# Kernel tuning notes

Hardware: AMD Instinct MI355X
Metric: run time of the kernel (lower is better)

Reference implementation:

```python
import jax, jax.numpy as jnp
import numpy as np

B, S, D_IN, D_OUT = 8, 2048, 768, 768

def setup_inputs() -> dict:
    key = jax.random.key(0)
    k1, k2 = jax.random.split(key)
    x = jax.random.normal(k1, (B, S, D_IN), dtype=jnp.float32)
    QKV = jax.random.normal(k2, (3, D_IN, D_OUT), dtype=jnp.float32) * 0.02
    return {"x": x, "QKV": QKV}

def reference(x, QKV):
    # Single-head self-attention; scale uses sqrt(d_in) as in the original.
    q = jnp.einsum('bsd,de->bse', x, QKV[0])  # [B,S,D_OUT]
    k = jnp.einsum('bsd,de->bse', x, QKV[1])
    v = jnp.einsum('bsd,de->bse', x, QKV[2])
    scale = 1.0 / jnp.sqrt(jnp.asarray(x.shape[-1], dtype=x.dtype))
    scores = jnp.einsum('bqe,bke->bqk', q, k) * scale  # [B,S,S]
    probs = jax.nn.softmax(scores, axis=-1)
    return jnp.einsum('bqk,bke->bqe', probs, v)  # [B,S,D_OUT]
```

## Files before the change

### kernel.cpp

```cpp
#include <hip/hip_runtime.h>
#include <hip/hip_bf16.h>
#include <cstdint>


#define NB 8
#define NS 2048
#define ND 768
#define NQK 1536
#define MTOT 16384

using f32x4 = __attribute__((ext_vector_type(4))) float;
using s16x8 = __attribute__((ext_vector_type(8))) short;

struct alignas(16) bf16x8 { __hip_bfloat16 h[8]; };
struct alignas(8)  bf16x4 { __hip_bfloat16 h[4]; };

#define CVT_BLOCKS 4096
#define WT_BLOCKS 1728
__global__ __launch_bounds__(256) void preprocess_kernel(const float* __restrict__ x,
                                                         __hip_bfloat16* __restrict__ xb,
                                                         const float* __restrict__ W,
                                                         __hip_bfloat16* __restrict__ Wt,
                                                         float* __restrict__ rowsum) {
    __shared__ float tile[32][33];
    const int tid = threadIdx.x;
    if (blockIdx.x < CVT_BLOCKS) {
#pragma unroll
        for (int it = 0; it < 3; ++it) {
            const int i = (it * CVT_BLOCKS + blockIdx.x) * 256 + tid;
            const f32x4 v = __builtin_nontemporal_load((const f32x4*)x + i);
            bf16x4 o;
            o.h[0] = __float2bfloat16(v[0]);
            o.h[1] = __float2bfloat16(v[1]);
            o.h[2] = __float2bfloat16(v[2]);
            o.h[3] = __float2bfloat16(v[3]);
            ((bf16x4*)xb)[i] = o;
        }
    } else if (blockIdx.x < CVT_BLOCKS + WT_BLOCKS) {
        const int bid = blockIdx.x - CVT_BLOCKS;
        const int e = bid / 576, rem = bid % 576;
        const int k0 = (rem / 24) * 32, n0 = (rem % 24) * 32;
        const float* Wp = W + (size_t)e * ND * ND;
        __hip_bfloat16* Wo = Wt + (size_t)e * ND * ND;
        {
            const int ty = tid >> 3, tx = tid & 7;
            const f32x4 v = __builtin_nontemporal_load(
                (const f32x4*)&Wp[(k0 + ty) * ND + n0 + tx * 4]);
#pragma unroll
            for (int q = 0; q < 4; ++q) tile[ty][tx * 4 + q] = v[q];
        }
        __syncthreads();
        {
            const int np = tid >> 3, kq = tid & 7;
            bf16x4 o;
#pragma unroll
            for (int q = 0; q < 4; ++q) o.h[q] = __float2bfloat16(tile[kq * 4 + q][np]);
            *(bf16x4*)&Wo[(long)(n0 + np) * ND + k0 + kq * 4] = o;
        }
    } else {
        const int i = (blockIdx.x - CVT_BLOCKS - WT_BLOCKS) * 1024 + tid * 4;
        f32x4 z = {0.f, 0.f, 0.f, 0.f};
        *(f32x4*)(rowsum + i) = z;
    }
}

__device__ __forceinline__ void storeC(float* p, float v) { *p = v; }
__device__ __forceinline__ void storeC(__hip_bfloat16* p, float v) { *p = __float2bfloat16(v); }

template <typename OutT, int EPI, bool BATCH_X>
__global__ __launch_bounds__(256, 3) void gemm_bt_kernel(
    const __hip_bfloat16* __restrict__ A,
    const __hip_bfloat16* __restrict__ Bm,
    OutT* __restrict__ C,
    __hip_bfloat16* __restrict__ vtOut,
    float* __restrict__ rowsum,
    int K, int lda, int ldb, int ldc,
    long sA, long sB, long sC, float scale) {
    __shared__ char smem[32768];
    char* AsB = smem;
    char* BsB = smem + 16384;

    int b, tileM, tileN;
    if (BATCH_X) {
        b = blockIdx.x; tileN = blockIdx.y * 128; tileM = blockIdx.z * 128;
    } else {
        b = blockIdx.z; tileN = blockIdx.x * 128; tileM = blockIdx.y * 128;
    }
    A  += (long)b * sA;
    Bm += (long)b * sB;
    C  += (long)b * sC;

    const int tid  = threadIdx.x;
    const int lane = tid & 63;
    const int wave = tid >> 6;
    const int wm = (wave >> 1) * 64;
    const int wn = (wave & 1) * 64;
    const int quad = lane >> 4;
    const int lrow = lane & 15;

    const int srow = tid >> 3;
    const int scol = ((tid & 7) ^ (srow & 7)) << 3;

    f32x4 acc[4][4];
    const f32x4 zero = {0.f, 0.f, 0.f, 0.f};
#pragma unroll
    for (int i = 0; i < 4; ++i)
#pragma unroll
        for (int j = 0; j < 4; ++j) acc[i][j] = zero;

    const __hip_bfloat16* gA = A + (long)(tileM + srow) * lda + scol;
    const __hip_bfloat16* gB = Bm + (long)(tileN + srow) * ldb + scol;
    const int ldsOff = tid * 16;

    typedef const __attribute__((address_space(1))) void* gp;
    typedef __attribute__((address_space(3))) void* sp;

    const int swa = (lrow & 7) << 4;

    for (int k0 = 0; k0 < K; k0 += 64) {
        __syncthreads();
#pragma unroll
        for (int j = 0; j < 4; ++j)
            __builtin_amdgcn_global_load_lds((gp)(gA + (long)(j * 32) * lda + k0),
                                             (sp)(AsB + j * 4096 + ldsOff), 16, 0, 0);
#pragma unroll
        for (int j = 0; j < 4; ++j)
            __builtin_amdgcn_global_load_lds((gp)(gB + (long)(j * 32) * ldb + k0),
                                             (sp)(BsB + j * 4096 + ldsOff), 16, 0, 0);
        __syncthreads();

#pragma unroll
        for (int kk = 0; kk < 2; ++kk) {
            s16x8 af[4], bfr[4];
#pragma unroll
            for (int i = 0; i < 4; ++i)
                af[i] = *(const s16x8*)(AsB + (wm + i * 16 + lrow) * 128 +
                                        ((((kk << 2) | quad) << 4) ^ swa));
#pragma unroll
            for (int j = 0; j < 4; ++j)
                bfr[j] = *(const s16x8*)(BsB + (wn + j * 16 + lrow) * 128 +
                                         ((((kk << 2) | quad) << 4) ^ swa));
#pragma unroll
            for (int i = 0; i < 4; ++i)
#pragma unroll
                for (int j = 0; j < 4; ++j)
                    acc[i][j] = __builtin_amdgcn_mfma_f32_16x16x32_bf16(af[i], bfr[j], acc[i][j], 0, 0, 0);
        }
    }

    if (EPI == 2 && tileN >= NQK) {
        __syncthreads();
        char* T = smem;
#pragma unroll
        for (int i = 0; i < 4; ++i) {
#pragma unroll
            for (int j = 0; j < 4; ++j) {
                const int d = wn + j * 16 + lrow;
                const int s = wm + i * 16 + quad * 4;
                bf16x4 g;
#pragma unroll
                for (int r = 0; r < 4; ++r) g.h[r] = __float2bfloat16(acc[i][j][r]);
                const int c = s >> 3;
                const int off = d * 256 + (((c ^ (d & 15)) << 4) | ((s & 4) << 1));
                *(bf16x4*)(T + off) = g;
            }
        }
        __syncthreads();
        const int dl = tid >> 1, half = tid & 1;
        const long bb = tileM >> 11;
        const int s0 = tileM & (NS - 1);
        const long dg = (long)(tileN - NQK) + dl;
        __hip_bfloat16* dst = vtOut + (bb * ND + dg) * NS + s0;
#pragma unroll
        for (int cc = 0; cc < 8; ++cc) {
            const int c2 = half * 8 + cc;
            s16x8 val = *(const s16x8*)(T + dl * 256 + ((c2 ^ (dl & 15)) << 4));
            *(s16x8*)(dst + c2 * 8) = val;
        }
        return;
    }

    if (EPI == 3) {
#pragma unroll
        for (int i = 0; i < 4; ++i) {
            float rs[4] = {0.f, 0.f, 0.f, 0.f};
#pragma unroll
            for (int j = 0; j < 4; ++j) {
                const int col = tileN + wn + j * 16 + lrow;
#pragma unroll
                for (int r = 0; r < 4; ++r) {
                    const int row = tileM + wm + i * 16 + quad * 4 + r;
                    const float e = __expf(acc[i][j][r] * scale);
                    const __hip_bfloat16 h = __float2bfloat16(e);
                    storeC(C + (long)row * ldc + col, __bfloat162float(h));
                    rs[r] += __bfloat162float(h);
                }
            }
#pragma unroll
            for (int r = 0; r < 4; ++r) {
#pragma unroll
                for (int off = 1; off < 16; off <<= 1) rs[r] += __shfl_xor(rs[r], off);
            }
            if (lrow == 0) {
#pragma unroll
                for (int r = 0; r < 4; ++r)
                    atomicAdd(rowsum + (long)b * NS + tileM + wm + i * 16 + quad * 4 + r, rs[r]);
            }
        }
        return;
    }

    if (EPI == 4) {
#pragma unroll
        for (int i = 0; i < 4; ++i) {
            float inv[4];
#pragma unroll
            for (int r = 0; r < 4; ++r)
                inv[r] = 1.0f / rowsum[(long)b * NS + tileM + wm + i * 16 + quad * 4 + r];
#pragma unroll
            for (int j = 0; j < 4; ++j) {
                const int col = tileN + wn + j * 16 + lrow;
#pragma unroll
                for (int r = 0; r < 4; ++r) {
                    const int row = tileM + wm + i * 16 + quad * 4 + r;
                    storeC(C + (long)row * ldc + col, acc[i][j][r] * inv[r]);
                }
            }
        }
        return;
    }

#pragma unroll
    for (int i = 0; i < 4; ++i) {
#pragma unroll
        for (int j = 0; j < 4; ++j) {
            const int col = tileN + wn + j * 16 + lrow;
#pragma unroll
            for (int r = 0; r < 4; ++r) {
                const int row = tileM + wm + i * 16 + quad * 4 + r;
                storeC(C + (long)row * ldc + col, acc[i][j][r] * scale);
            }
        }
    }
}

extern "C" void kernel_launch(void* const* d_in, const int* in_sizes, int n_in,
                              void* d_out, int out_size, void* d_ws, size_t ws_size,
                              hipStream_t stream) {
    const float* x   = (const float*)d_in[0];
    const float* QKV = (const float*)d_in[1];
    float* out = (float*)d_out;

    uint8_t* ws = (uint8_t*)d_ws;
    constexpr size_t XB_BYTES  = (size_t)MTOT * ND * 2;
    constexpr size_t WT_BYTES  = (size_t)3 * ND * ND * 2;
    constexpr size_t QKV_BYTES = (size_t)MTOT * NQK * 2;
    constexpr size_t VT_BYTES  = (size_t)NB * ND * NS * 2;
    constexpr size_t PR_BYTES  = (size_t)MTOT * NS * 2;
    __hip_bfloat16* xb    = (__hip_bfloat16*)(ws);
    __hip_bfloat16* Wt    = (__hip_bfloat16*)(ws + XB_BYTES);
    __hip_bfloat16* qkvb  = (__hip_bfloat16*)(ws + XB_BYTES + WT_BYTES);
    __hip_bfloat16* vt    = (__hip_bfloat16*)(ws + XB_BYTES + WT_BYTES + QKV_BYTES);
    __hip_bfloat16* probs = (__hip_bfloat16*)(ws + XB_BYTES + WT_BYTES + QKV_BYTES + VT_BYTES);
    float*          rowsum= (float*)(ws + XB_BYTES + WT_BYTES + QKV_BYTES + VT_BYTES + PR_BYTES);

    const float scale = 0.03608439182435161f;

    preprocess_kernel<<<CVT_BLOCKS + WT_BLOCKS + 16, 256, 0, stream>>>(x, xb, QKV, Wt, rowsum);
    gemm_bt_kernel<__hip_bfloat16, 2, false><<<dim3(2304 / 128, MTOT / 128, 1), 256, 0, stream>>>(
        xb, Wt, qkvb, vt, nullptr, ND, ND, ND, NQK, 0, 0, 0, 1.0f);
    gemm_bt_kernel<__hip_bfloat16, 3, true><<<dim3(NB, NS / 128, NS / 128), 256, 0, stream>>>(
        qkvb, qkvb + ND, probs, nullptr, rowsum, ND, NQK, NQK, NS,
        (long)NS * NQK, (long)NS * NQK, (long)NS * NS, scale);
    gemm_bt_kernel<float, 4, true><<<dim3(NB, ND / 128, NS / 128), 256, 0, stream>>>(
        probs, vt, out, nullptr, rowsum, NS, NS, NS, ND,
        (long)NS * NS, (long)ND * NS, (long)NS * ND, 1.0f);
}
```

Baseline: 286.2 us.

## Replace 128x128 GEMM with 256x256 double-buffered pipelined 8-wave kernel

All three GEMMs now use 256x256 tiles computed by 512 threads, with 128KB LDS double buffering. Async global-to-LDS loads for the next K-tiles are interleaved with MFMA quarters using explicit waitcnt, s_barrier and setprio scheduling. The QKV projection also remaps blocks into eight interleaved groups to improve L2 locality. This targets exposed load latency and per-tile synchronisation overhead, at the cost of higher register pressure, one block per CU-class occupancy, and fewer blocks (e.g. 192 for the PV GEMM), which can leave the GPU underfilled.

```diff
diff --git a/kernel.cpp b/kernel.cpp
--- a/kernel.cpp
+++ b/kernel.cpp
@@ -67,24 +67,114 @@
 __device__ __forceinline__ void storeC(float* p, float v) { *p = v; }
 __device__ __forceinline__ void storeC(__hip_bfloat16* p, float v) { *p = __float2bfloat16(v); }
 
-template <typename OutT, int EPI, bool BATCH_X>
-__global__ __launch_bounds__(256, 3) void gemm_bt_kernel(
+typedef const __attribute__((address_space(1))) void* gp;
+typedef __attribute__((address_space(3))) void* sp;
+
+#define SBAR() asm volatile("s_barrier" ::: "memory")
+
+#define STAGE_AH(H_, T_) do {                                                              \
+    char* d_ = smem + (((T_) & 1) * 65536) + (H_) * 16384 + ldsOff;                        \
+    __builtin_amdgcn_global_load_lds((gp)(gA + (long)((H_) * 128) * lda + (T_) * 64),      \
+                                     (sp)d_, 16, 0, 0);                                    \
+    __builtin_amdgcn_global_load_lds((gp)(gA + (long)((H_) * 128 + 64) * lda + (T_) * 64), \
+                                     (sp)(d_ + 8192), 16, 0, 0);                           \
+} while (0)
+
+#define STAGE_BH(H_, T_) do {                                                              \
+    char* d_ = smem + (((T_) & 1) * 65536) + 32768 + (H_) * 16384 + ldsOff;                \
+    __builtin_amdgcn_global_load_lds((gp)(gB + (long)((H_) * 128) * ldb + (T_) * 64),      \
+                                     (sp)d_, 16, 0, 0);                                    \
+    __builtin_amdgcn_global_load_lds((gp)(gB + (long)((H_) * 128 + 64) * ldb + (T_) * 64), \
+                                     (sp)(d_ + 8192), 16, 0, 0);                           \
+} while (0)
+
+#define MFMA_Q(MI0_, NI0_) do {                                                            \
+    _Pragma("unroll") for (int m_ = 0; m_ < 4; ++m_)                                       \
+    _Pragma("unroll") for (int n_ = 0; n_ < 2; ++n_)                                       \
+    _Pragma("unroll") for (int k_ = 0; k_ < 2; ++k_)                                       \
+        acc[(MI0_) + m_][(NI0_) + n_] = __builtin_amdgcn_mfma_f32_16x16x32_bf16(           \
+            af[m_][k_], bf[(NI0_) + n_][k_], acc[(MI0_) + m_][(NI0_) + n_], 0, 0, 0);      \
+} while (0)
+
+#define KTILE(T_, SP1_, SP3_, SP4_, VM_) do {                                              \
+    char* abase = smem + (((T_) & 1) * 65536);                                             \
+    char* bbase = abase + 32768;                                                           \
+                  \
+    _Pragma("unroll") for (int m_ = 0; m_ < 4; ++m_) {                                     \
+        af[m_][0] = *(const s16x8*)(abase + aoff + m_ * 2048 + ck0);                       \
+        af[m_][1] = *(const s16x8*)(abase + aoff + m_ * 2048 + ck1);                       \
+    }                                                                                      \
+    _Pragma("unroll") for (int n_ = 0; n_ < 2; ++n_) {                                     \
+        bf[n_][0] = *(const s16x8*)(bbase + boff + n_ * 2048 + ck0);                       \
+        bf[n_][1] = *(const s16x8*)(bbase + boff + n_ * 2048 + ck1);                       \
+    }                                                                                      \
+    if (SP1_) STAGE_AH(1, (T_) + 1);                                                       \
+    asm volatile("s_waitcnt lgkmcnt(8)" ::: "memory");                                     \
+    SBAR();                                                                                \
+    asm volatile("s_waitcnt lgkmcnt(0)" ::: "memory");                                     \
+    __builtin_amdgcn_sched_barrier(0);                                                     \
+    __builtin_amdgcn_s_setprio(1);                                                         \
+    MFMA_Q(0, 0);                                                                          \
+    __builtin_amdgcn_s_setprio(0);                                                         \
+    SBAR();                                                                                \
+           \
+    _Pragma("unroll") for (int n_ = 0; n_ < 2; ++n_) {                                     \
+        bf[2 + n_][0] = *(const s16x8*)(bbase + boff + (2 + n_) * 2048 + ck0);             \
+        bf[2 + n_][1] = *(const s16x8*)(bbase + boff + (2 + n_) * 2048 + ck1);             \
+    }                                                                                      \
+    SBAR();                                                                                \
+    asm volatile("s_waitcnt lgkmcnt(0)" ::: "memory");                                     \
+    __builtin_amdgcn_sched_barrier(0);                                                     \
+    __builtin_amdgcn_s_setprio(1);                                                         \
+    MFMA_Q(0, 2);                                                                          \
+    __builtin_amdgcn_s_setprio(0);                                                         \
+    SBAR();                                                                                \
+           \
+    _Pragma("unroll") for (int m_ = 0; m_ < 4; ++m_) {                                     \
+        af[m_][0] = *(const s16x8*)(abase + aoff + (4 + m_) * 2048 + ck0);                 \
+        af[m_][1] = *(const s16x8*)(abase + aoff + (4 + m_) * 2048 + ck1);                 \
+    }                                                                                      \
+    if (SP3_) STAGE_BH(0, (T_) + 2);                                                       \
+    SBAR();                                                                                \
+    asm volatile("s_waitcnt lgkmcnt(0)" ::: "memory");                                     \
+    __builtin_amdgcn_sched_barrier(0);                                                     \
+    __builtin_amdgcn_s_setprio(1);                                                         \
+    MFMA_Q(4, 2);                                                                          \
+    __builtin_amdgcn_s_setprio(0);                                                         \
+    SBAR();                                                                                \
+            \
+    if (SP4_) { STAGE_AH(0, (T_) + 2); STAGE_BH(1, (T_) + 2); }                            \
+    if ((VM_) == 0) { asm volatile("s_waitcnt vmcnt(6)" ::: "memory"); }                   \
+    else if ((VM_) == 1) { asm volatile("s_waitcnt vmcnt(0)" ::: "memory"); }              \
+    SBAR();                                                                                \
+    __builtin_amdgcn_s_setprio(1);                                                         \
+    MFMA_Q(4, 0);                                                                          \
+    __builtin_amdgcn_s_setprio(0);                                                         \
+    SBAR();                                                                                \
+} while (0)
+
+template <typename OutT, int EPI, int NKT, bool BATCH_X>
+__global__ __launch_bounds__(512, 2) void gemm256_kernel(
     const __hip_bfloat16* __restrict__ A,
     const __hip_bfloat16* __restrict__ Bm,
     OutT* __restrict__ C,
     __hip_bfloat16* __restrict__ vtOut,
     float* __restrict__ rowsum,
-    int K, int lda, int ldb, int ldc,
+    int lda, int ldb, int ldc,
     long sA, long sB, long sC, float scale) {
-    __shared__ char smem[32768];
-    char* AsB = smem;
-    char* BsB = smem + 16384;
+    static_assert(NKT >= 3, "pipeline needs >= 3 K-tiles");
+    __shared__ alignas(16) char smem[131072];
 
     int b, tileM, tileN;
     if (BATCH_X) {
-        b = blockIdx.x; tileN = blockIdx.y * 128; tileM = blockIdx.z * 128;
+        b = blockIdx.x; tileN = blockIdx.y * 256; tileM = blockIdx.z * 256;
     } else {
-        b = blockIdx.z; tileN = blockIdx.x * 128; tileM = blockIdx.y * 128;
+        b = 0;
+        const int l0 = blockIdx.y * gridDim.x + blockIdx.x;
+        const int cpx = (gridDim.x * gridDim.y) >> 3;
+        const int tl = (l0 & 7) * cpx + (l0 >> 3);
+        tileN = (tl % gridDim.x) * 256;
+        tileM = (tl / gridDim.x) * 256;
     }
     A  += (long)b * sA;
     Bm += (long)b * sB;
@@ -92,76 +182,55 @@
 
     const int tid  = threadIdx.x;
     const int lane = tid & 63;
-    const int wave = tid >> 6;
-    const int wm = (wave >> 1) * 64;
-    const int wn = (wave & 1) * 64;
+    const int wid  = tid >> 6;
+    const int wr   = wid >> 2;
+    const int wc   = wid & 3;
     const int quad = lane >> 4;
     const int lrow = lane & 15;
 
     const int srow = tid >> 3;
     const int scol = ((tid & 7) ^ (srow & 7)) << 3;
-
-    f32x4 acc[4][4];
-    const f32x4 zero = {0.f, 0.f, 0.f, 0.f};
-#pragma unroll
-    for (int i = 0; i < 4; ++i)
-#pragma unroll
-        for (int j = 0; j < 4; ++j) acc[i][j] = zero;
-
     const __hip_bfloat16* gA = A + (long)(tileM + srow) * lda + scol;
     const __hip_bfloat16* gB = Bm + (long)(tileN + srow) * ldb + scol;
     const int ldsOff = tid * 16;
 
-    typedef const __attribute__((address_space(1))) void* gp;
-    typedef __attribute__((address_space(3))) void* sp;
-
-    const int swa = (lrow & 7) << 4;
-
-    for (int k0 = 0; k0 < K; k0 += 64) {
-        __syncthreads();
-#pragma unroll
-        for (int j = 0; j < 4; ++j)
-            __builtin_amdgcn_global_load_lds((gp)(gA + (long)(j * 32) * lda + k0),
-                                             (sp)(AsB + j * 4096 + ldsOff), 16, 0, 0);
-#pragma unroll
-        for (int j = 0; j < 4; ++j)
-            __builtin_amdgcn_global_load_lds((gp)(gB + (long)(j * 32) * ldb + k0),
-                                             (sp)(BsB + j * 4096 + ldsOff), 16, 0, 0);
-        __syncthreads();
-
-#pragma unroll
-        for (int kk = 0; kk < 2; ++kk) {
-            s16x8 af[4], bfr[4];
-#pragma unroll
-            for (int i = 0; i < 4; ++i)
-                af[i] = *(const s16x8*)(AsB + (wm + i * 16 + lrow) * 128 +
-                                        ((((kk << 2) | quad) << 4) ^ swa));
-#pragma unroll
-            for (int j = 0; j < 4; ++j)
-                bfr[j] = *(const s16x8*)(BsB + (wn + j * 16 + lrow) * 128 +
-                                         ((((kk << 2) | quad) << 4) ^ swa));
-#pragma unroll
-            for (int i = 0; i < 4; ++i)
-#pragma unroll
-                for (int j = 0; j < 4; ++j)
-                    acc[i][j] = __builtin_amdgcn_mfma_f32_16x16x32_bf16(af[i], bfr[j], acc[i][j], 0, 0, 0);
-        }
-    }
+    const int swa  = lrow & 7;
+    const int ck0  = (quad ^ swa) << 4;
+    const int ck1  = ((quad + 4) ^ swa) << 4;
+    const int aoff = wr * 16384 + lrow * 128;
+    const int boff = wc * 8192 + lrow * 128;
+
+    f32x4 acc[8][4];
+    const f32x4 zero = {0.f, 0.f, 0.f, 0.f};
+#pragma unroll
+    for (int i = 0; i < 8; ++i)
+#pragma unroll
+        for (int j = 0; j < 4; ++j) acc[i][j] = zero;
+
+    STAGE_AH(0, 0); STAGE_BH(0, 0); STAGE_BH(1, 0); STAGE_AH(1, 0);
+    asm volatile("s_waitcnt vmcnt(4)" ::: "memory");
+    STAGE_AH(0, 1); STAGE_BH(0, 1); STAGE_BH(1, 1);
+    asm volatile("s_waitcnt vmcnt(6)" ::: "memory");
+    SBAR();
+
+    s16x8 af[4][2], bf[4][2];
+#pragma unroll 1
+    for (int t = 0; t < NKT - 2; ++t) { KTILE(t, 1, 1, 1, 0); }
+    KTILE(NKT - 2, 1, 0, 0, 1);
+    KTILE(NKT - 1, 0, 0, 0, 2);
 
     if (EPI == 2 && tileN >= NQK) {
-        __syncthreads();
         char* T = smem;
 #pragma unroll
-        for (int i = 0; i < 4; ++i) {
-#pragma unroll
-            for (int j = 0; j < 4; ++j) {
-                const int d = wn + j * 16 + lrow;
-                const int s = wm + i * 16 + quad * 4;
+        for (int mi = 0; mi < 8; ++mi) {
+#pragma unroll
+            for (int ni = 0; ni < 4; ++ni) {
+                const int d = wc * 64 + ni * 16 + lrow;
+                const int s = wr * 128 + mi * 16 + quad * 4;
                 bf16x4 g;
 #pragma unroll
-                for (int r = 0; r < 4; ++r) g.h[r] = __float2bfloat16(acc[i][j][r]);
-                const int c = s >> 3;
-                const int off = d * 256 + (((c ^ (d & 15)) << 4) | ((s & 4) << 1));
+                for (int r = 0; r < 4; ++r) g.h[r] = __float2bfloat16(acc[mi][ni][r]);
+                const int off = d * 512 + ((((s >> 3) ^ (d & 31)) << 4) | ((s & 4) << 1));
                 *(bf16x4*)(T + off) = g;
             }
         }
@@ -172,9 +241,9 @@
         const long dg = (long)(tileN - NQK) + dl;
         __hip_bfloat16* dst = vtOut + (bb * ND + dg) * NS + s0;
 #pragma unroll
-        for (int cc = 0; cc < 8; ++cc) {
-            const int c2 = half * 8 + cc;
-            s16x8 val = *(const s16x8*)(T + dl * 256 + ((c2 ^ (dl & 15)) << 4));
+        for (int cc = 0; cc < 16; ++cc) {
+            const int c2 = half * 16 + cc;
+            s16x8 val = *(const s16x8*)(T + dl * 512 + ((c2 ^ (dl & 31)) << 4));
             *(s16x8*)(dst + c2 * 8) = val;
         }
         return;
@@ -182,15 +251,15 @@
 
     if (EPI == 3) {
 #pragma unroll
-        for (int i = 0; i < 4; ++i) {
+        for (int mi = 0; mi < 8; ++mi) {
             float rs[4] = {0.f, 0.f, 0.f, 0.f};
 #pragma unroll
-            for (int j = 0; j < 4; ++j) {
-                const int col = tileN + wn + j * 16 + lrow;
+            for (int ni = 0; ni < 4; ++ni) {
+                const int col = tileN + wc * 64 + ni * 16 + lrow;
 #pragma unroll
                 for (int r = 0; r < 4; ++r) {
-                    const int row = tileM + wm + i * 16 + quad * 4 + r;
-                    const float e = __expf(acc[i][j][r] * scale);
+                    const int row = tileM + wr * 128 + mi * 16 + quad * 4 + r;
+                    const float e = __expf(acc[mi][ni][r] * scale);
                     const __hip_bfloat16 h = __float2bfloat16(e);
                     storeC(C + (long)row * ldc + col, __bfloat162float(h));
                     rs[r] += __bfloat162float(h);
@@ -204,7 +273,8 @@
             if (lrow == 0) {
 #pragma unroll
                 for (int r = 0; r < 4; ++r)
-                    atomicAdd(rowsum + (long)b * NS + tileM + wm + i * 16 + quad * 4 + r, rs[r]);
+                    atomicAdd(rowsum + (long)b * NS + tileM + wr * 128 + mi * 16 + quad * 4 + r,
+                              rs[r]);
             }
         }
         return;
@@ -212,18 +282,18 @@
 
     if (EPI == 4) {
 #pragma unroll
-        for (int i = 0; i < 4; ++i) {
+        for (int mi = 0; mi < 8; ++mi) {
             float inv[4];
 #pragma unroll
             for (int r = 0; r < 4; ++r)
-                inv[r] = 1.0f / rowsum[(long)b * NS + tileM + wm + i * 16 + quad * 4 + r];
-#pragma unroll
-            for (int j = 0; j < 4; ++j) {
-                const int col = tileN + wn + j * 16 + lrow;
+                inv[r] = 1.0f / rowsum[(long)b * NS + tileM + wr * 128 + mi * 16 + quad * 4 + r];
+#pragma unroll
+            for (int ni = 0; ni < 4; ++ni) {
+                const int col = tileN + wc * 64 + ni * 16 + lrow;
 #pragma unroll
                 for (int r = 0; r < 4; ++r) {
-                    const int row = tileM + wm + i * 16 + quad * 4 + r;
-                    storeC(C + (long)row * ldc + col, acc[i][j][r] * inv[r]);
+                    const int row = tileM + wr * 128 + mi * 16 + quad * 4 + r;
+                    storeC(C + (long)row * ldc + col, acc[mi][ni][r] * inv[r]);
                 }
             }
         }
@@ -231,14 +301,14 @@
     }
 
 #pragma unroll
-    for (int i = 0; i < 4; ++i) {
-#pragma unroll
-        for (int j = 0; j < 4; ++j) {
-            const int col = tileN + wn + j * 16 + lrow;
+    for (int mi = 0; mi < 8; ++mi) {
+#pragma unroll
+        for (int ni = 0; ni < 4; ++ni) {
+            const int col = tileN + wc * 64 + ni * 16 + lrow;
 #pragma unroll
             for (int r = 0; r < 4; ++r) {
-                const int row = tileM + wm + i * 16 + quad * 4 + r;
-                storeC(C + (long)row * ldc + col, acc[i][j][r] * scale);
+                const int row = tileM + wr * 128 + mi * 16 + quad * 4 + r;
+                storeC(C + (long)row * ldc + col, acc[mi][ni][r] * scale);
             }
         }
     }
@@ -267,12 +337,12 @@
     const float scale = 0.03608439182435161f;
 
     preprocess_kernel<<<CVT_BLOCKS + WT_BLOCKS + 16, 256, 0, stream>>>(x, xb, QKV, Wt, rowsum);
-    gemm_bt_kernel<__hip_bfloat16, 2, false><<<dim3(2304 / 128, MTOT / 128, 1), 256, 0, stream>>>(
-        xb, Wt, qkvb, vt, nullptr, ND, ND, ND, NQK, 0, 0, 0, 1.0f);
-    gemm_bt_kernel<__hip_bfloat16, 3, true><<<dim3(NB, NS / 128, NS / 128), 256, 0, stream>>>(
-        qkvb, qkvb + ND, probs, nullptr, rowsum, ND, NQK, NQK, NS,
+    gemm256_kernel<__hip_bfloat16, 2, 12, false><<<dim3(2304 / 256, MTOT / 256, 1), 512, 0, stream>>>(
+        xb, Wt, qkvb, vt, nullptr, ND, ND, NQK, 0, 0, 0, 1.0f);
+    gemm256_kernel<__hip_bfloat16, 3, 12, true><<<dim3(NB, NS / 256, NS / 256), 512, 0, stream>>>(
+        qkvb, qkvb + ND, probs, nullptr, rowsum, NQK, NQK, NS,
         (long)NS * NQK, (long)NS * NQK, (long)NS * NS, scale);
-    gemm_bt_kernel<float, 4, true><<<dim3(NB, ND / 128, NS / 128), 256, 0, stream>>>(
-        probs, vt, out, nullptr, rowsum, NS, NS, NS, ND,
+    gemm256_kernel<float, 4, 32, true><<<dim3(NB, ND / 256, NS / 256), 512, 0, stream>>>(
+        probs, vt, out, nullptr, rowsum, NS, NS, ND,
         (long)NS * NS, (long)ND * NS, (long)NS * ND, 1.0f);
 }
```

Result: slower. 295.3 us (+3.2%).
